# Kernel optimization log

Hardware: AMD Instinct MI355X
Metric: run time of the kernel (lower is better)

The kernel has to match this reference:

```python
import jax, jax.numpy as jnp
import numpy as np

B, S, DIM = 2, 2048, 2048
H, DK, DR, DC, DCP, DV = 16, 128, 64, 512, 1024, 128


def setup_inputs() -> dict:
    key = jax.random.key(0)
    ks = jax.random.split(key, 8)
    s = 0.02  # weight init scale
    return {
        "x": jax.random.normal(ks[0], (B, S, DIM), jnp.float32),
        "W_c": jax.random.normal(ks[1], (DIM, DC), jnp.float32) * s,
        "W_c_prime": jax.random.normal(ks[2], (DIM, DCP), jnp.float32) * s,
        "W_qc": jax.random.normal(ks[3], (H, DCP, DK), jnp.float32) * s,
        "W_qr": jax.random.normal(ks[4], (H, DCP, DR), jnp.float32) * s,
        "W_kc": jax.random.normal(ks[5], (H, DC, DK), jnp.float32) * s,
        "W_kr": jax.random.normal(ks[6], (DIM, DR), jnp.float32) * s,
        "W_v": jax.random.normal(ks[7], (H, DC, DV), jnp.float32) * s,
    }


def reference(x, W_c, W_c_prime, W_qc, W_qr, W_kc, W_kr, W_v):
    # Latent compressions
    c = x @ W_c                 # [B,S,DC]  compressed KV latent
    cp = x @ W_c_prime          # [B,S,DCP] compressed Q latent
    # Per-head projections, vectorized over heads
    q_c = jnp.einsum('bsc,hck->bhsk', cp, W_qc)   # [B,H,S,DK]
    q_r = jnp.einsum('bsc,hcr->bhsr', cp, W_qr)   # [B,H,S,DR]
    k_c = jnp.einsum('bsc,hck->bhsk', c, W_kc)    # [B,H,S,DK]
    k_r = x @ W_kr                                 # [B,S,DR] shared across heads
    q = jnp.concatenate([q_c, q_r], axis=-1)                               # [B,H,S,DK+DR]
    k = jnp.concatenate([k_c, jnp.broadcast_to(k_r[:, None], (B, H, S, DR))], axis=-1)
    scale = 1.0 / np.sqrt(DK + DR)
    scores = jnp.einsum('bhsd,bhtd->bhst', q, k) * scale                   # [B,H,S,S]
    causal = jnp.tril(jnp.ones((S, S), dtype=bool))
    scores = jnp.where(causal, scores, -jnp.inf)
    probs = jax.nn.softmax(scores.astype(jnp.float32), axis=-1).astype(q.dtype)
    v = jnp.einsum('bsc,hcv->bhsv', c, W_v)                                # [B,H,S,DV]
    out = jnp.einsum('bhst,bhtv->bhsv', probs, v)                          # [B,H,S,DV]
    return out.transpose(0, 2, 1, 3).reshape(B, S, H * DV)                 # concat heads
```

## Files before the change

kernel.cpp:

```cpp
#include <hip/hip_runtime.h>
#include <stdint.h>

typedef __bf16 bf16;
typedef __bf16 bfx8 __attribute__((ext_vector_type(8)));
typedef __bf16 bfx4 __attribute__((ext_vector_type(4)));
typedef float floatx4 __attribute__((ext_vector_type(4)));

#define B_ 2
#define S_ 2048
#define DIM_ 2048
#define H_ 16
#define DK_ 128
#define DR_ 64
#define DC_ 512
#define DCP_ 1024
#define DV_ 128
#define DQK_ 192

#define MASK_VAL (-30000.0f)
#define C1_ 0.10411754f

__global__ void k_cast(const float* __restrict__ in, bf16* __restrict__ out) {
    size_t i = ((size_t)blockIdx.x * 256 + threadIdx.x) * 8;
    float4 a = *(const float4*)(in + i);
    float4 b = *(const float4*)(in + i + 4);
    bfx8 r;
    r[0] = (bf16)a.x; r[1] = (bf16)a.y; r[2] = (bf16)a.z; r[3] = (bf16)a.w;
    r[4] = (bf16)b.x; r[5] = (bf16)b.y; r[6] = (bf16)b.z; r[7] = (bf16)b.w;
    *(bfx8*)(out + i) = r;
}

__global__ void k_transpose(const float* __restrict__ in, bf16* __restrict__ out,
                            int K, int N) {
    __shared__ float tile[32][33];
    int h = blockIdx.z;
    int n0 = blockIdx.x * 32, k0 = blockIdx.y * 32;
    const float* ip = in + (size_t)h * K * N;
    bf16* op = out + (size_t)h * K * N;
    int tx = threadIdx.x & 31, ty = threadIdx.x >> 5;
#pragma unroll
    for (int i = 0; i < 32; i += 8)
        tile[ty + i][tx] = ip[(size_t)(k0 + ty + i) * N + (n0 + tx)];
    __syncthreads();
#pragma unroll
    for (int i = 0; i < 32; i += 8)
        op[(size_t)(n0 + ty + i) * K + (k0 + tx)] = (bf16)tile[tx][ty + i];
}

__device__ __forceinline__ void gld16(const bf16* g, bf16* l) {
    __builtin_amdgcn_global_load_lds(
        (const __attribute__((address_space(1))) void*)g,
        (__attribute__((address_space(3))) void*)l, 16, 0, 0);
}

__device__ __forceinline__ bfx8 frag_ld(const bf16* lds, int row, int quad) {
    int pb = quad ^ ((row >> 1) & 3);
    return *(const bfx8*)(lds + row * 32 + pb * 8);
}

#define SLICE_ 4096

__device__ __forceinline__ void gemm_core(const bf16* __restrict__ A,
                                          const bf16* __restrict__ Bt,
                                          int K, int rowlimB,
                                          floatx4 acc[4][4],
                                          bf16* A_lds, bf16* B_lds) {
    int tid = threadIdx.x, wave = tid >> 6, lane = tid & 63;
    int l15 = lane & 15, quad = lane >> 4;
    int wm = (wave & 1) * 64, wn = (wave >> 1) * 64;
    int ch0 = wave * 2, ch1 = wave * 2 + 1;
    int r0 = ch0 * 16 + (lane >> 2), r1 = ch1 * 16 + (lane >> 2);
    int kb0 = (lane & 3) ^ ((r0 >> 1) & 3), kb1 = (lane & 3) ^ ((r1 >> 1) & 3);
    int rb0 = r0 <= rowlimB ? r0 : rowlimB;
    int rb1 = r1 <= rowlimB ? r1 : rowlimB;
    const bf16* a0 = A + (size_t)r0 * K + kb0 * 8;
    const bf16* a1 = A + (size_t)r1 * K + kb1 * 8;
    const bf16* b0 = Bt + (size_t)rb0 * K + kb0 * 8;
    const bf16* b1 = Bt + (size_t)rb1 * K + kb1 * 8;
    bf16* da0 = A_lds + ch0 * 512;
    bf16* da1 = A_lds + ch1 * 512;
    bf16* db0 = B_lds + ch0 * 512;
    bf16* db1 = B_lds + ch1 * 512;
    for (int k0 = 0; k0 < K; k0 += 64) {
        __syncthreads();
        gld16(a0 + k0, da0);
        gld16(a1 + k0, da1);
        gld16(b0 + k0, db0);
        gld16(b1 + k0, db1);
        gld16(a0 + k0 + 32, da0 + SLICE_);
        gld16(a1 + k0 + 32, da1 + SLICE_);
        gld16(b0 + k0 + 32, db0 + SLICE_);
        gld16(b1 + k0 + 32, db1 + SLICE_);
        __syncthreads();
#pragma unroll
        for (int sl = 0; sl < 2; ++sl) {
            const bf16* As = A_lds + sl * SLICE_;
            const bf16* Bs = B_lds + sl * SLICE_;
            bfx8 a[4], b[4];
#pragma unroll
            for (int t = 0; t < 4; ++t) a[t] = frag_ld(As, wm + t * 16 + l15, quad);
#pragma unroll
            for (int t = 0; t < 4; ++t) b[t] = frag_ld(Bs, wn + t * 16 + l15, quad);
#pragma unroll
            for (int mt = 0; mt < 4; ++mt)
#pragma unroll
                for (int nt = 0; nt < 4; ++nt)
                    acc[mt][nt] = __builtin_amdgcn_mfma_f32_16x16x32_bf16(
                        a[mt], b[nt], acc[mt][nt], 0, 0, 0);
        }
    }
}

__global__ __launch_bounds__(256, 3) void k_gemm1(
    const bf16* __restrict__ xb, const bf16* __restrict__ Wt_c,
    const bf16* __restrict__ Wt_cp, const bf16* __restrict__ Wt_kr,
    bf16* __restrict__ c_ws, bf16* __restrict__ cp_ws, bf16* __restrict__ kr_ws) {
    __shared__ __attribute__((aligned(16))) bf16 A_lds[2 * SLICE_];
    __shared__ __attribute__((aligned(16))) bf16 B_lds[2 * SLICE_];
    int bx = blockIdx.x, by = blockIdx.y;
    const bf16* Bt; bf16* outp; int ldc, col0, rowlim;
    if (bx < 4)       { Bt = Wt_c  + (size_t)bx * 128 * DIM_;       outp = c_ws;  ldc = DC_;  col0 = bx * 128;       rowlim = 127; }
    else if (bx < 12) { Bt = Wt_cp + (size_t)(bx - 4) * 128 * DIM_; outp = cp_ws; ldc = DCP_; col0 = (bx - 4) * 128; rowlim = 127; }
    else              { Bt = Wt_kr;                                  outp = kr_ws; ldc = DR_;  col0 = 0;              rowlim = 63;  }
    floatx4 acc[4][4];
#pragma unroll
    for (int i = 0; i < 4; ++i)
#pragma unroll
        for (int j = 0; j < 4; ++j) acc[i][j] = (floatx4){0.f, 0.f, 0.f, 0.f};
    gemm_core(xb + (size_t)by * 128 * DIM_, Bt, DIM_, rowlim, acc, A_lds, B_lds);
    int tid = threadIdx.x, wave = tid >> 6, lane = tid & 63;
    int l15 = lane & 15, quad = lane >> 4;
    int wm = (wave & 1) * 64, wn = (wave >> 1) * 64;
#pragma unroll
    for (int mt = 0; mt < 4; ++mt)
#pragma unroll
        for (int nt = 0; nt < 4; ++nt) {
            int n = wn + nt * 16 + l15;
            if (n > rowlim) continue;
#pragma unroll
            for (int r = 0; r < 4; ++r) {
                int m = by * 128 + wm + mt * 16 + quad * 4 + r;
                outp[(size_t)m * ldc + col0 + n] = (bf16)acc[mt][nt][r];
            }
        }
}

__global__ __launch_bounds__(256, 3) void k_gemm2(
    const bf16* __restrict__ cp_ws, const bf16* __restrict__ Wt_qc,
    const bf16* __restrict__ Wt_qr, bf16* __restrict__ q_ws) {
    __shared__ __attribute__((aligned(16))) bf16 A_lds[2 * SLICE_];
    __shared__ __attribute__((aligned(16))) bf16 B_lds[2 * SLICE_];
    int bx = blockIdx.x, by = blockIdx.y, h = blockIdx.z;
    const bf16* Bt; int col0, rowlim;
    if (bx == 0) { Bt = Wt_qc + (size_t)h * DK_ * DCP_; col0 = 0;   rowlim = 127; }
    else         { Bt = Wt_qr + (size_t)h * DR_ * DCP_; col0 = 128; rowlim = 63;  }
    floatx4 acc[4][4];
#pragma unroll
    for (int i = 0; i < 4; ++i)
#pragma unroll
        for (int j = 0; j < 4; ++j) acc[i][j] = (floatx4){0.f, 0.f, 0.f, 0.f};
    gemm_core(cp_ws + (size_t)by * 128 * DCP_, Bt, DCP_, rowlim, acc, A_lds, B_lds);
    int tid = threadIdx.x, wave = tid >> 6, lane = tid & 63;
    int l15 = lane & 15, quad = lane >> 4;
    int wm = (wave & 1) * 64, wn = (wave >> 1) * 64;
#pragma unroll
    for (int mt = 0; mt < 4; ++mt)
#pragma unroll
        for (int nt = 0; nt < 4; ++nt) {
            int n = wn + nt * 16 + l15;
            if (n > rowlim) continue;
#pragma unroll
            for (int r = 0; r < 4; ++r) {
                int m = by * 128 + wm + mt * 16 + quad * 4 + r;
                int b = m >> 11, s = m & 2047;
                q_ws[(((size_t)b * H_ + h) * S_ + s) * DQK_ + col0 + n] =
                    (bf16)(acc[mt][nt][r] * C1_);
            }
        }
}

__global__ __launch_bounds__(256, 3) void k_gemm3(
    const bf16* __restrict__ c_ws, const bf16* __restrict__ Wt_kc,
    const bf16* __restrict__ Wt_v, bf16* __restrict__ kc_ws, bf16* __restrict__ vt_ws) {
    __shared__ __attribute__((aligned(16))) bf16 A_lds[2 * SLICE_];
    __shared__ __attribute__((aligned(16))) bf16 B_lds[2 * SLICE_];
    int bx = blockIdx.x, by = blockIdx.y, h = blockIdx.z;
    const bf16* Bt = (bx == 0) ? (Wt_kc + (size_t)h * DK_ * DC_)
                               : (Wt_v  + (size_t)h * DV_ * DC_);
    floatx4 acc[4][4];
#pragma unroll
    for (int i = 0; i < 4; ++i)
#pragma unroll
        for (int j = 0; j < 4; ++j) acc[i][j] = (floatx4){0.f, 0.f, 0.f, 0.f};
    gemm_core(c_ws + (size_t)by * 128 * DC_, Bt, DC_, 127, acc, A_lds, B_lds);
    int tid = threadIdx.x, wave = tid >> 6, lane = tid & 63;
    int l15 = lane & 15, quad = lane >> 4;
    int wm = (wave & 1) * 64, wn = (wave >> 1) * 64;
#pragma unroll
    for (int mt = 0; mt < 4; ++mt)
#pragma unroll
        for (int nt = 0; nt < 4; ++nt) {
            int n = wn + nt * 16 + l15;
            if (bx == 0) {
#pragma unroll
                for (int r = 0; r < 4; ++r) {
                    int m = by * 128 + wm + mt * 16 + quad * 4 + r;
                    int b = m >> 11, s = m & 2047;
                    kc_ws[(((size_t)b * H_ + h) * S_ + s) * DK_ + n] = (bf16)acc[mt][nt][r];
                }
            } else {
                int m0 = by * 128 + wm + mt * 16 + quad * 4;
                int b = m0 >> 11, s = m0 & 2047;
                bfx4 pack;
#pragma unroll
                for (int r = 0; r < 4; ++r) pack[r] = (bf16)acc[mt][nt][r];
                *(bfx4*)(&vt_ws[(((size_t)b * H_ + h) * DV_ + n) * S_ + s]) = pack;
            }
        }
}

#define KSTR 200
#define VSTR 72
#define PSTR 72

__global__ __launch_bounds__(256, 2) void k_attn(
    const bf16* __restrict__ q_ws, const bf16* __restrict__ kc_ws,
    const bf16* __restrict__ kr_ws, const bf16* __restrict__ vt_ws,
    float* __restrict__ out) {
    __shared__ __attribute__((aligned(16))) bf16 K_lds[64 * KSTR];
    __shared__ __attribute__((aligned(16))) bf16 V_lds[128 * VSTR];
    __shared__ __attribute__((aligned(16))) bf16 P_lds[64 * PSTR];
    int p = blockIdx.x;
    int bh = blockIdx.y, b = bh >> 4, h = bh & 15;
    int tid = threadIdx.x, wave = tid >> 6, lane = tid & 63;
    int l15 = lane & 15, quad = lane >> 4;

    bf16 ov = (bf16)(l15 == 0 ? 1.f : 0.f);
    bfx8 ones8 = {ov, ov, ov, ov, ov, ov, ov, ov};

    int kn[4], kcc[4], rn[2], rcc[2], vr[4], vcc[4];
#pragma unroll
    for (int i = 0; i < 4; ++i) { int f = (i * 256 + tid) * 8; kn[i] = f >> 7; kcc[i] = f & 127; }
#pragma unroll
    for (int i = 0; i < 2; ++i) { int f = (i * 256 + tid) * 8; rn[i] = f >> 6; rcc[i] = f & 63; }
#pragma unroll
    for (int i = 0; i < 4; ++i) { int f = (i * 256 + tid) * 8; vr[i] = f >> 6; vcc[i] = f & 63; }
    const bf16* kcp[4]; const bf16* krp[2]; const bf16* vp[4];
#pragma unroll
    for (int i = 0; i < 4; ++i) kcp[i] = kc_ws + ((size_t)bh * S_ + kn[i]) * DK_ + kcc[i];
#pragma unroll
    for (int i = 0; i < 2; ++i) krp[i] = kr_ws + ((size_t)b * S_ + rn[i]) * DR_ + rcc[i];
#pragma unroll
    for (int i = 0; i < 4; ++i) vp[i] = vt_ws + ((size_t)bh * DV_ + vr[i]) * S_ + vcc[i];

    for (int ph = 0; ph < 2; ++ph) {
        int qt = ph ? p : 31 - p;
        int q0 = qt * 64, ntiles = qt + 1;

        const bf16* qrow = q_ws + ((size_t)bh * S_ + q0 + wave * 16 + l15) * DQK_;
        bfx8 qf[6];
#pragma unroll
        for (int ks = 0; ks < 6; ++ks)
            qf[ks] = *(const bfx8*)(qrow + ks * 32 + quad * 8);

        floatx4 o_acc[9];
#pragma unroll
        for (int vt = 0; vt < 9; ++vt) o_acc[vt] = (floatx4){0.f, 0.f, 0.f, 0.f};

        bfx8 pk[4], pr[2], pv[4];
#pragma unroll
        for (int i = 0; i < 4; ++i) pk[i] = *(const bfx8*)(kcp[i]);
#pragma unroll
        for (int i = 0; i < 2; ++i) pr[i] = *(const bfx8*)(krp[i]);
#pragma unroll
        for (int i = 0; i < 4; ++i) pv[i] = *(const bfx8*)(vp[i]);

        for (int t = 0; t < ntiles; ++t) {
            __syncthreads();
#pragma unroll
            for (int i = 0; i < 4; ++i) *(bfx8*)(&K_lds[kn[i] * KSTR + kcc[i]]) = pk[i];
#pragma unroll
            for (int i = 0; i < 2; ++i) *(bfx8*)(&K_lds[rn[i] * KSTR + 128 + rcc[i]]) = pr[i];
#pragma unroll
            for (int i = 0; i < 4; ++i) *(bfx8*)(&V_lds[vr[i] * VSTR + vcc[i]]) = pv[i];
            __syncthreads();
            if (t + 1 < ntiles) {
                size_t kv1 = (size_t)(t + 1) * 64;
#pragma unroll
                for (int i = 0; i < 4; ++i) pk[i] = *(const bfx8*)(kcp[i] + kv1 * DK_);
#pragma unroll
                for (int i = 0; i < 2; ++i) pr[i] = *(const bfx8*)(krp[i] + kv1 * DR_);
#pragma unroll
                for (int i = 0; i < 4; ++i) pv[i] = *(const bfx8*)(vp[i] + kv1);
            }
            floatx4 sc[4];
#pragma unroll
            for (int nt = 0; nt < 4; ++nt) sc[nt] = (floatx4){0.f, 0.f, 0.f, 0.f};
            __builtin_amdgcn_s_setprio(1);
#pragma unroll
            for (int ks = 0; ks < 6; ++ks)
#pragma unroll
                for (int nt = 0; nt < 4; ++nt) {
                    bfx8 kf = *(const bfx8*)(&K_lds[(nt * 16 + l15) * KSTR + ks * 32 + quad * 8]);
                    sc[nt] = __builtin_amdgcn_mfma_f32_16x16x32_bf16(qf[ks], kf, sc[nt], 0, 0, 0);
                }
            __builtin_amdgcn_s_setprio(0);
            if (t == ntiles - 1) {
                int kv0 = t * 64;
#pragma unroll
                for (int nt = 0; nt < 4; ++nt)
#pragma unroll
                    for (int r = 0; r < 4; ++r) {
                        int n_g = kv0 + nt * 16 + l15;
                        int q_g = q0 + wave * 16 + quad * 4 + r;
                        if (n_g > q_g) sc[nt][r] = MASK_VAL;
                    }
            }
#pragma unroll
            for (int nt = 0; nt < 4; ++nt)
#pragma unroll
                for (int r = 0; r < 4; ++r)
                    P_lds[(wave * 16 + quad * 4 + r) * PSTR + nt * 16 + l15] =
                        (bf16)exp2f(sc[nt][r]);
            __builtin_amdgcn_s_setprio(1);
#pragma unroll
            for (int ks2 = 0; ks2 < 2; ++ks2) {
                bfx8 pf = *(const bfx8*)(&P_lds[(wave * 16 + l15) * PSTR + ks2 * 32 + quad * 8]);
#pragma unroll
                for (int vt = 0; vt < 8; ++vt) {
                    bfx8 vf = *(const bfx8*)(&V_lds[(vt * 16 + l15) * VSTR + ks2 * 32 + quad * 8]);
                    o_acc[vt] = __builtin_amdgcn_mfma_f32_16x16x32_bf16(pf, vf, o_acc[vt], 0, 0, 0);
                }
                o_acc[8] = __builtin_amdgcn_mfma_f32_16x16x32_bf16(pf, ones8, o_acc[8], 0, 0, 0);
            }
            __builtin_amdgcn_s_setprio(0);
        }
        float rinv[4];
#pragma unroll
        for (int r = 0; r < 4; ++r)
            rinv[r] = 1.f / __shfl(o_acc[8][r], lane & 48);
#pragma unroll
        for (int vt = 0; vt < 8; ++vt)
#pragma unroll
            for (int r = 0; r < 4; ++r) {
                int s = q0 + wave * 16 + quad * 4 + r;
                int v = vt * 16 + l15;
                out[((size_t)b * S_ + s) * (H_ * DV_) + h * DV_ + v] = o_acc[vt][r] * rinv[r];
            }
    }
}

extern "C" void kernel_launch(void* const* d_in, const int* in_sizes, int n_in,
                              void* d_out, int out_size, void* d_ws, size_t ws_size,
                              hipStream_t stream) {
    const float* x    = (const float*)d_in[0];
    const float* W_c  = (const float*)d_in[1];
    const float* W_cp = (const float*)d_in[2];
    const float* W_qc = (const float*)d_in[3];
    const float* W_qr = (const float*)d_in[4];
    const float* W_kc = (const float*)d_in[5];
    const float* W_kr = (const float*)d_in[6];
    const float* W_v  = (const float*)d_in[7];
    float* out = (float*)d_out;

    bf16* c_ws  = (bf16*)d_out;
    bf16* cp_ws = c_ws + (size_t)B_ * S_ * DC_;
    bf16* xb    = cp_ws + (size_t)B_ * S_ * DCP_;

    char* ws = (char*)d_ws;
    size_t off = 0;
    auto alloc = [&](size_t elems) { bf16* p = (bf16*)(ws + off); off += elems * sizeof(bf16); return p; };
    bf16* Wt_c  = alloc((size_t)DIM_ * DC_);
    bf16* Wt_cp = alloc((size_t)DIM_ * DCP_);
    bf16* Wt_qc = alloc((size_t)H_ * DCP_ * DK_);
    bf16* Wt_qr = alloc((size_t)H_ * DCP_ * DR_);
    bf16* Wt_kc = alloc((size_t)H_ * DC_ * DK_);
    bf16* Wt_kr = alloc((size_t)DIM_ * DR_);
    bf16* Wt_v  = alloc((size_t)H_ * DC_ * DV_);
    bf16* kr_ws = alloc((size_t)B_ * S_ * DR_);
    bf16* q_ws  = alloc((size_t)B_ * H_ * S_ * DQK_);
    bf16* kc_ws = alloc((size_t)B_ * H_ * S_ * DK_);
    bf16* vt_ws = alloc((size_t)B_ * H_ * DV_ * S_);

    k_cast<<<dim3(4096), 256, 0, stream>>>(x, xb);
    k_transpose<<<dim3(DC_ / 32, DIM_ / 32, 1),  256, 0, stream>>>(W_c,  Wt_c,  DIM_, DC_);
    k_transpose<<<dim3(DCP_ / 32, DIM_ / 32, 1), 256, 0, stream>>>(W_cp, Wt_cp, DIM_, DCP_);
    k_transpose<<<dim3(DK_ / 32, DCP_ / 32, H_), 256, 0, stream>>>(W_qc, Wt_qc, DCP_, DK_);
    k_transpose<<<dim3(DR_ / 32, DCP_ / 32, H_), 256, 0, stream>>>(W_qr, Wt_qr, DCP_, DR_);
    k_transpose<<<dim3(DK_ / 32, DC_ / 32, H_),  256, 0, stream>>>(W_kc, Wt_kc, DC_, DK_);
    k_transpose<<<dim3(DR_ / 32, DIM_ / 32, 1),  256, 0, stream>>>(W_kr, Wt_kr, DIM_, DR_);
    k_transpose<<<dim3(DV_ / 32, DC_ / 32, H_),  256, 0, stream>>>(W_v,  Wt_v,  DC_, DV_);

    k_gemm1<<<dim3(13, 32), 256, 0, stream>>>(xb, Wt_c, Wt_cp, Wt_kr, c_ws, cp_ws, kr_ws);
    k_gemm2<<<dim3(2, 32, H_), 256, 0, stream>>>(cp_ws, Wt_qc, Wt_qr, q_ws);
    k_gemm3<<<dim3(2, 32, H_), 256, 0, stream>>>(c_ws, Wt_kc, Wt_v, kc_ws, vt_ws);
    k_attn<<<dim3(16, B_ * H_), 256, 0, stream>>>(q_ws, kc_ws, kr_ws, vt_ws, out);
}
```

Before: 324.1 us.

## Fuse weight transposes, pack qr heads in gemm2, split attention query tiles

All seven weight transposes now run as one launch that picks its matrix from the block index, which removes six kernel launches. gemm2 computes two heads' 64-wide qr projections in a single 128-wide tile, so no tile wastes half its MMA work. Attention now launches one block per query tile with the largest tiles first, instead of pairing two tiles per block to balance work. It also raises occupancy to 3 blocks per CU and shrinks the P stride, relying on the hardware scheduler to handle the uneven causal work and accepting possible LDS bank conflicts from the new stride.

```diff
diff --git a/kernel.cpp b/kernel.cpp
--- a/kernel.cpp
+++ b/kernel.cpp
@@ -30,11 +30,28 @@
     *(bfx8*)(out + i) = r;
 }
 
-__global__ void k_transpose(const float* __restrict__ in, bf16* __restrict__ out,
-                            int K, int N) {
+__global__ void k_transpose_all(
+    const float* __restrict__ W_c, const float* __restrict__ W_cp,
+    const float* __restrict__ W_qc, const float* __restrict__ W_qr,
+    const float* __restrict__ W_kc, const float* __restrict__ W_kr,
+    const float* __restrict__ W_v,
+    bf16* __restrict__ Wt_c, bf16* __restrict__ Wt_cp,
+    bf16* __restrict__ Wt_qc, bf16* __restrict__ Wt_qr,
+    bf16* __restrict__ Wt_kc, bf16* __restrict__ Wt_kr,
+    bf16* __restrict__ Wt_v) {
     __shared__ float tile[32][33];
-    int h = blockIdx.z;
-    int n0 = blockIdx.x * 32, k0 = blockIdx.y * 32;
+    int bid = blockIdx.x;
+    const float* in; bf16* out; int K, N, lx, ly, local;
+    if (bid < 1024)      { in = W_c;  out = Wt_c;  K = 2048; N = 512;  lx = 4; ly = 6; local = bid; }
+    else if (bid < 3072) { in = W_cp; out = Wt_cp; K = 2048; N = 1024; lx = 5; ly = 6; local = bid - 1024; }
+    else if (bid < 5120) { in = W_qc; out = Wt_qc; K = 1024; N = 128;  lx = 2; ly = 5; local = bid - 3072; }
+    else if (bid < 6144) { in = W_qr; out = Wt_qr; K = 1024; N = 64;   lx = 1; ly = 5; local = bid - 5120; }
+    else if (bid < 7168) { in = W_kc; out = Wt_kc; K = 512;  N = 128;  lx = 2; ly = 4; local = bid - 6144; }
+    else if (bid < 7296) { in = W_kr; out = Wt_kr; K = 2048; N = 64;   lx = 1; ly = 6; local = bid - 7168; }
+    else                 { in = W_v;  out = Wt_v;  K = 512;  N = 128;  lx = 2; ly = 4; local = bid - 7296; }
+    int n0 = (local & ((1 << lx) - 1)) << 5;
+    int k0 = ((local >> lx) & ((1 << ly) - 1)) << 5;
+    int h  = local >> (lx + ly);
     const float* ip = in + (size_t)h * K * N;
     bf16* op = out + (size_t)h * K * N;
     int tx = threadIdx.x & 31, ty = threadIdx.x >> 5;
@@ -150,16 +167,16 @@
     const bf16* __restrict__ Wt_qr, bf16* __restrict__ q_ws) {
     __shared__ __attribute__((aligned(16))) bf16 A_lds[2 * SLICE_];
     __shared__ __attribute__((aligned(16))) bf16 B_lds[2 * SLICE_];
-    int bx = blockIdx.x, by = blockIdx.y, h = blockIdx.z;
-    const bf16* Bt; int col0, rowlim;
-    if (bx == 0) { Bt = Wt_qc + (size_t)h * DK_ * DCP_; col0 = 0;   rowlim = 127; }
-    else         { Bt = Wt_qr + (size_t)h * DR_ * DCP_; col0 = 128; rowlim = 63;  }
+    int bx = blockIdx.x, by = blockIdx.y, hz = blockIdx.z;
+    const bf16* Bt;
+    if (bx < 2) Bt = Wt_qc + (size_t)(hz * 2 + bx) * DK_ * DCP_;
+    else        Bt = Wt_qr + (size_t)hz * 128 * DCP_;
     floatx4 acc[4][4];
 #pragma unroll
     for (int i = 0; i < 4; ++i)
 #pragma unroll
         for (int j = 0; j < 4; ++j) acc[i][j] = (floatx4){0.f, 0.f, 0.f, 0.f};
-    gemm_core(cp_ws + (size_t)by * 128 * DCP_, Bt, DCP_, rowlim, acc, A_lds, B_lds);
+    gemm_core(cp_ws + (size_t)by * 128 * DCP_, Bt, DCP_, 127, acc, A_lds, B_lds);
     int tid = threadIdx.x, wave = tid >> 6, lane = tid & 63;
     int l15 = lane & 15, quad = lane >> 4;
     int wm = (wave & 1) * 64, wn = (wave >> 1) * 64;
@@ -168,12 +185,14 @@
 #pragma unroll
         for (int nt = 0; nt < 4; ++nt) {
             int n = wn + nt * 16 + l15;
-            if (n > rowlim) continue;
+            int h, col;
+            if (bx < 2) { h = hz * 2 + bx;        col = n; }
+            else        { h = hz * 2 + (n >> 6);  col = 128 + (n & 63); }
 #pragma unroll
             for (int r = 0; r < 4; ++r) {
                 int m = by * 128 + wm + mt * 16 + quad * 4 + r;
                 int b = m >> 11, s = m & 2047;
-                q_ws[(((size_t)b * H_ + h) * S_ + s) * DQK_ + col0 + n] =
+                q_ws[(((size_t)b * H_ + h) * S_ + s) * DQK_ + col] =
                     (bf16)(acc[mt][nt][r] * C1_);
             }
         }
@@ -221,16 +240,16 @@
 
 #define KSTR 200
 #define VSTR 72
-#define PSTR 72
-
-__global__ __launch_bounds__(256, 2) void k_attn(
+#define PSTR 68
+
+__global__ __launch_bounds__(256, 3) void k_attn(
     const bf16* __restrict__ q_ws, const bf16* __restrict__ kc_ws,
     const bf16* __restrict__ kr_ws, const bf16* __restrict__ vt_ws,
     float* __restrict__ out) {
     __shared__ __attribute__((aligned(16))) bf16 K_lds[64 * KSTR];
     __shared__ __attribute__((aligned(16))) bf16 V_lds[128 * VSTR];
     __shared__ __attribute__((aligned(16))) bf16 P_lds[64 * PSTR];
-    int p = blockIdx.x;
+    int qt = 31 - (int)blockIdx.x;
     int bh = blockIdx.y, b = bh >> 4, h = bh & 15;
     int tid = threadIdx.x, wave = tid >> 6, lane = tid & 63;
     int l15 = lane & 15, quad = lane >> 4;
@@ -253,101 +272,98 @@
 #pragma unroll
     for (int i = 0; i < 4; ++i) vp[i] = vt_ws + ((size_t)bh * DV_ + vr[i]) * S_ + vcc[i];
 
-    for (int ph = 0; ph < 2; ++ph) {
-        int qt = ph ? p : 31 - p;
-        int q0 = qt * 64, ntiles = qt + 1;
-
-        const bf16* qrow = q_ws + ((size_t)bh * S_ + q0 + wave * 16 + l15) * DQK_;
-        bfx8 qf[6];
+    int q0 = qt * 64, ntiles = qt + 1;
+
+    const bf16* qrow = q_ws + ((size_t)bh * S_ + q0 + wave * 16 + l15) * DQK_;
+    bfx8 qf[6];
+#pragma unroll
+    for (int ks = 0; ks < 6; ++ks)
+        qf[ks] = *(const bfx8*)(qrow + ks * 32 + quad * 8);
+
+    floatx4 o_acc[9];
+#pragma unroll
+    for (int vt = 0; vt < 9; ++vt) o_acc[vt] = (floatx4){0.f, 0.f, 0.f, 0.f};
+
+    bfx8 pk[4], pr[2], pv[4];
+#pragma unroll
+    for (int i = 0; i < 4; ++i) pk[i] = *(const bfx8*)(kcp[i]);
+#pragma unroll
+    for (int i = 0; i < 2; ++i) pr[i] = *(const bfx8*)(krp[i]);
+#pragma unroll
+    for (int i = 0; i < 4; ++i) pv[i] = *(const bfx8*)(vp[i]);
+
+    for (int t = 0; t < ntiles; ++t) {
+        __syncthreads();
+#pragma unroll
+        for (int i = 0; i < 4; ++i) *(bfx8*)(&K_lds[kn[i] * KSTR + kcc[i]]) = pk[i];
+#pragma unroll
+        for (int i = 0; i < 2; ++i) *(bfx8*)(&K_lds[rn[i] * KSTR + 128 + rcc[i]]) = pr[i];
+#pragma unroll
+        for (int i = 0; i < 4; ++i) *(bfx8*)(&V_lds[vr[i] * VSTR + vcc[i]]) = pv[i];
+        __syncthreads();
+        if (t + 1 < ntiles) {
+            size_t kv1 = (size_t)(t + 1) * 64;
+#pragma unroll
+            for (int i = 0; i < 4; ++i) pk[i] = *(const bfx8*)(kcp[i] + kv1 * DK_);
+#pragma unroll
+            for (int i = 0; i < 2; ++i) pr[i] = *(const bfx8*)(krp[i] + kv1 * DR_);
+#pragma unroll
+            for (int i = 0; i < 4; ++i) pv[i] = *(const bfx8*)(vp[i] + kv1);
+        }
+        floatx4 sc[4];
+#pragma unroll
+        for (int nt = 0; nt < 4; ++nt) sc[nt] = (floatx4){0.f, 0.f, 0.f, 0.f};
+        __builtin_amdgcn_s_setprio(1);
 #pragma unroll
         for (int ks = 0; ks < 6; ++ks)
-            qf[ks] = *(const bfx8*)(qrow + ks * 32 + quad * 8);
-
-        floatx4 o_acc[9];
-#pragma unroll
-        for (int vt = 0; vt < 9; ++vt) o_acc[vt] = (floatx4){0.f, 0.f, 0.f, 0.f};
-
-        bfx8 pk[4], pr[2], pv[4];
-#pragma unroll
-        for (int i = 0; i < 4; ++i) pk[i] = *(const bfx8*)(kcp[i]);
-#pragma unroll
-        for (int i = 0; i < 2; ++i) pr[i] = *(const bfx8*)(krp[i]);
-#pragma unroll
-        for (int i = 0; i < 4; ++i) pv[i] = *(const bfx8*)(vp[i]);
-
-        for (int t = 0; t < ntiles; ++t) {
-            __syncthreads();
-#pragma unroll
-            for (int i = 0; i < 4; ++i) *(bfx8*)(&K_lds[kn[i] * KSTR + kcc[i]]) = pk[i];
-#pragma unroll
-            for (int i = 0; i < 2; ++i) *(bfx8*)(&K_lds[rn[i] * KSTR + 128 + rcc[i]]) = pr[i];
-#pragma unroll
-            for (int i = 0; i < 4; ++i) *(bfx8*)(&V_lds[vr[i] * VSTR + vcc[i]]) = pv[i];
-            __syncthreads();
-            if (t + 1 < ntiles) {
-                size_t kv1 = (size_t)(t + 1) * 64;
-#pragma unroll
-                for (int i = 0; i < 4; ++i) pk[i] = *(const bfx8*)(kcp[i] + kv1 * DK_);
-#pragma unroll
-                for (int i = 0; i < 2; ++i) pr[i] = *(const bfx8*)(krp[i] + kv1 * DR_);
-#pragma unroll
-                for (int i = 0; i < 4; ++i) pv[i] = *(const bfx8*)(vp[i] + kv1);
+#pragma unroll
+            for (int nt = 0; nt < 4; ++nt) {
+                bfx8 kf = *(const bfx8*)(&K_lds[(nt * 16 + l15) * KSTR + ks * 32 + quad * 8]);
+                sc[nt] = __builtin_amdgcn_mfma_f32_16x16x32_bf16(qf[ks], kf, sc[nt], 0, 0, 0);
             }
-            floatx4 sc[4];
-#pragma unroll
-            for (int nt = 0; nt < 4; ++nt) sc[nt] = (floatx4){0.f, 0.f, 0.f, 0.f};
-            __builtin_amdgcn_s_setprio(1);
-#pragma unroll
-            for (int ks = 0; ks < 6; ++ks)
-#pragma unroll
-                for (int nt = 0; nt < 4; ++nt) {
-                    bfx8 kf = *(const bfx8*)(&K_lds[(nt * 16 + l15) * KSTR + ks * 32 + quad * 8]);
-                    sc[nt] = __builtin_amdgcn_mfma_f32_16x16x32_bf16(qf[ks], kf, sc[nt], 0, 0, 0);
+        __builtin_amdgcn_s_setprio(0);
+        if (t == ntiles - 1) {
+            int kv0 = t * 64;
+#pragma unroll
+            for (int nt = 0; nt < 4; ++nt)
+#pragma unroll
+                for (int r = 0; r < 4; ++r) {
+                    int n_g = kv0 + nt * 16 + l15;
+                    int q_g = q0 + wave * 16 + quad * 4 + r;
+                    if (n_g > q_g) sc[nt][r] = MASK_VAL;
                 }
-            __builtin_amdgcn_s_setprio(0);
-            if (t == ntiles - 1) {
-                int kv0 = t * 64;
-#pragma unroll
-                for (int nt = 0; nt < 4; ++nt)
-#pragma unroll
-                    for (int r = 0; r < 4; ++r) {
-                        int n_g = kv0 + nt * 16 + l15;
-                        int q_g = q0 + wave * 16 + quad * 4 + r;
-                        if (n_g > q_g) sc[nt][r] = MASK_VAL;
-                    }
+        }
+#pragma unroll
+        for (int nt = 0; nt < 4; ++nt)
+#pragma unroll
+            for (int r = 0; r < 4; ++r)
+                P_lds[(wave * 16 + quad * 4 + r) * PSTR + nt * 16 + l15] =
+                    (bf16)exp2f(sc[nt][r]);
+        __builtin_amdgcn_s_setprio(1);
+#pragma unroll
+        for (int ks2 = 0; ks2 < 2; ++ks2) {
+            bfx8 pf = *(const bfx8*)(&P_lds[(wave * 16 + l15) * PSTR + ks2 * 32 + quad * 8]);
+#pragma unroll
+            for (int vt = 0; vt < 8; ++vt) {
+                bfx8 vf = *(const bfx8*)(&V_lds[(vt * 16 + l15) * VSTR + ks2 * 32 + quad * 8]);
+                o_acc[vt] = __builtin_amdgcn_mfma_f32_16x16x32_bf16(pf, vf, o_acc[vt], 0, 0, 0);
             }
-#pragma unroll
-            for (int nt = 0; nt < 4; ++nt)
-#pragma unroll
-                for (int r = 0; r < 4; ++r)
-                    P_lds[(wave * 16 + quad * 4 + r) * PSTR + nt * 16 + l15] =
-                        (bf16)exp2f(sc[nt][r]);
-            __builtin_amdgcn_s_setprio(1);
-#pragma unroll
-            for (int ks2 = 0; ks2 < 2; ++ks2) {
-                bfx8 pf = *(const bfx8*)(&P_lds[(wave * 16 + l15) * PSTR + ks2 * 32 + quad * 8]);
-#pragma unroll
-                for (int vt = 0; vt < 8; ++vt) {
-                    bfx8 vf = *(const bfx8*)(&V_lds[(vt * 16 + l15) * VSTR + ks2 * 32 + quad * 8]);
-                    o_acc[vt] = __builtin_amdgcn_mfma_f32_16x16x32_bf16(pf, vf, o_acc[vt], 0, 0, 0);
-                }
-                o_acc[8] = __builtin_amdgcn_mfma_f32_16x16x32_bf16(pf, ones8, o_acc[8], 0, 0, 0);
-            }
-            __builtin_amdgcn_s_setprio(0);
-        }
-        float rinv[4];
-#pragma unroll
-        for (int r = 0; r < 4; ++r)
-            rinv[r] = 1.f / __shfl(o_acc[8][r], lane & 48);
-#pragma unroll
-        for (int vt = 0; vt < 8; ++vt)
-#pragma unroll
-            for (int r = 0; r < 4; ++r) {
-                int s = q0 + wave * 16 + quad * 4 + r;
-                int v = vt * 16 + l15;
-                out[((size_t)b * S_ + s) * (H_ * DV_) + h * DV_ + v] = o_acc[vt][r] * rinv[r];
-            }
+            o_acc[8] = __builtin_amdgcn_mfma_f32_16x16x32_bf16(pf, ones8, o_acc[8], 0, 0, 0);
+        }
+        __builtin_amdgcn_s_setprio(0);
     }
+    float rinv[4];
+#pragma unroll
+    for (int r = 0; r < 4; ++r)
+        rinv[r] = 1.f / __shfl(o_acc[8][r], lane & 48);
+#pragma unroll
+    for (int vt = 0; vt < 8; ++vt)
+#pragma unroll
+        for (int r = 0; r < 4; ++r) {
+            int s = q0 + wave * 16 + quad * 4 + r;
+            int v = vt * 16 + l15;
+            out[((size_t)b * S_ + s) * (H_ * DV_) + h * DV_ + v] = o_acc[vt][r] * rinv[r];
+        }
 }
 
 extern "C" void kernel_launch(void* const* d_in, const int* in_sizes, int n_in,
@@ -383,16 +399,12 @@
     bf16* vt_ws = alloc((size_t)B_ * H_ * DV_ * S_);
 
     k_cast<<<dim3(4096), 256, 0, stream>>>(x, xb);
-    k_transpose<<<dim3(DC_ / 32, DIM_ / 32, 1),  256, 0, stream>>>(W_c,  Wt_c,  DIM_, DC_);
-    k_transpose<<<dim3(DCP_ / 32, DIM_ / 32, 1), 256, 0, stream>>>(W_cp, Wt_cp, DIM_, DCP_);
-    k_transpose<<<dim3(DK_ / 32, DCP_ / 32, H_), 256, 0, stream>>>(W_qc, Wt_qc, DCP_, DK_);
-    k_transpose<<<dim3(DR_ / 32, DCP_ / 32, H_), 256, 0, stream>>>(W_qr, Wt_qr, DCP_, DR_);
-    k_transpose<<<dim3(DK_ / 32, DC_ / 32, H_),  256, 0, stream>>>(W_kc, Wt_kc, DC_, DK_);
-    k_transpose<<<dim3(DR_ / 32, DIM_ / 32, 1),  256, 0, stream>>>(W_kr, Wt_kr, DIM_, DR_);
-    k_transpose<<<dim3(DV_ / 32, DC_ / 32, H_),  256, 0, stream>>>(W_v,  Wt_v,  DC_, DV_);
+    k_transpose_all<<<dim3(8320), 256, 0, stream>>>(
+        W_c, W_cp, W_qc, W_qr, W_kc, W_kr, W_v,
+        Wt_c, Wt_cp, Wt_qc, Wt_qr, Wt_kc, Wt_kr, Wt_v);
 
     k_gemm1<<<dim3(13, 32), 256, 0, stream>>>(xb, Wt_c, Wt_cp, Wt_kr, c_ws, cp_ws, kr_ws);
-    k_gemm2<<<dim3(2, 32, H_), 256, 0, stream>>>(cp_ws, Wt_qc, Wt_qr, q_ws);
+    k_gemm2<<<dim3(3, 32, 8), 256, 0, stream>>>(cp_ws, Wt_qc, Wt_qr, q_ws);
     k_gemm3<<<dim3(2, 32, H_), 256, 0, stream>>>(c_ws, Wt_kc, Wt_v, kc_ws, vt_ws);
-    k_attn<<<dim3(16, B_ * H_), 256, 0, stream>>>(q_ws, kc_ws, kr_ws, vt_ws, out);
-}
+    k_attn<<<dim3(32, B_ * H_), 256, 0, stream>>>(q_ws, kc_ws, kr_ws, vt_ws, out);
+}
```

Measured after the change: 380.1 us. +17.3%, slower.
